# Kernel optimization log

Hardware: AMD Instinct MI355X
Metric: run time of the kernel (lower is better)

The kernel has to match this reference:

```python
import jax, jax.numpy as jnp
import numpy as np

H = 4096
IN = 512
OUT = 64


def setup_inputs() -> dict:
    key = jax.random.key(0)
    ks = jax.random.split(key, 10)
    return {
        "inp": jax.random.normal(ks[0], (1, IN), jnp.float32),
        "hidden": jax.random.normal(ks[1], (1, H), jnp.float32),
        "hebb": jax.random.normal(ks[2], (H, H), jnp.float32) * 0.01,
        "W_i2h": jax.random.normal(ks[3], (H, IN), jnp.float32) * (1.0 / np.sqrt(IN)),
        "b_i2h": jax.random.normal(ks[4], (H,), jnp.float32),
        "w": jax.random.uniform(ks[5], (H, H), jnp.float32) * 0.01,
        "plas": jax.random.uniform(ks[6], (H, H), jnp.float32) * 0.01,
        "learn": jnp.full((1,), 0.01, jnp.float32),
        "W_h2o": jax.random.normal(ks[7], (OUT, H), jnp.float32) * (1.0 / np.sqrt(H)),
        "b_h2o": jax.random.normal(ks[8], (OUT,), jnp.float32),
    }


def reference(inp, hidden, hebb, W_i2h, b_i2h, w, plas, learn, W_h2o, b_h2o):
    # plastic-Miconi, rule='hebb', activ='relu'
    # x = relu(i2h(input) + hidden @ (w + plas * hebb))   [1, H]
    pre = inp @ W_i2h.T + b_i2h + hidden @ (w + plas * hebb)
    x = jax.nn.relu(pre)
    # hebb <- (1 - learn) * hebb + learn * outer(hidden, x)   [H, H]
    hebb_new = (1.0 - learn) * hebb + learn * (hidden.T @ x)
    # output = tanh(h2o(x))   [1, OUT]
    out = jnp.tanh(x @ W_h2o.T + b_h2o)
    return out, x, hebb_new
```

## Files before the change

### kernel.cpp

```cpp
#include <hip/hip_runtime.h>
#include <math.h>

#define H 4096
#define INP 512
#define OUTN 64
#define H4 (H / 4)
#define SPLITS 1024
#define ROWS (H / SPLITS)

typedef float v4f __attribute__((ext_vector_type(4)));

__global__ __launch_bounds__(256) void k_partial(
    const float* __restrict__ hidden,
    const float* __restrict__ w,
    const float* __restrict__ plas,
    const float* __restrict__ hebb,
    float* __restrict__ partial)
{
    const int col4 = blockIdx.x * 256 + threadIdx.x;
    const int i0   = blockIdx.y * ROWS;
    const float4* __restrict__ w4 = (const float4*)w;
    const float4* __restrict__ p4 = (const float4*)plas;
    const float4* __restrict__ h4 = (const float4*)hebb;

    float4 wv[ROWS], pv[ROWS], hb[ROWS];
#pragma unroll
    for (int r = 0; r < ROWS; ++r) {
        const size_t idx = (size_t)(i0 + r) * H4 + col4;
        wv[r] = w4[idx];
        pv[r] = p4[idx];
        hb[r] = h4[idx];
    }
    float4 acc = make_float4(0.f, 0.f, 0.f, 0.f);
#pragma unroll
    for (int r = 0; r < ROWS; ++r) {
        const float hv = hidden[i0 + r];
        acc.x += hv * (wv[r].x + pv[r].x * hb[r].x);
        acc.y += hv * (wv[r].y + pv[r].y * hb[r].y);
        acc.z += hv * (wv[r].z + pv[r].z * hb[r].z);
        acc.w += hv * (wv[r].w + pv[r].w * hb[r].w);
    }
    ((float4*)partial)[(size_t)blockIdx.y * H4 + col4] = acc;
}

__global__ __launch_bounds__(256) void k_finish_x(
    const float* __restrict__ partial,
    const float* __restrict__ inp,
    const float* __restrict__ W_i2h,
    const float* __restrict__ b_i2h,
    float* __restrict__ x_out)
{
    const int t  = threadIdx.x;
    const int j0 = blockIdx.x * 16;
    const int jj = t & 15;
    const int sg = t >> 4;

    float sum = 0.f;
    for (int s = sg; s < SPLITS; s += 16)
        sum += partial[(size_t)s * H + j0 + jj];

    __shared__ float red[16][17];
    red[sg][jj] = sum;
    __syncthreads();

    const int wave = t >> 6;
    const int lane = t & 63;
    const float4* __restrict__ in4 = (const float4*)inp;

#pragma unroll
    for (int q = 0; q < 4; ++q) {
        const int jj2 = wave * 4 + q;
        const int j = j0 + jj2;
        const float4* __restrict__ row4 = (const float4*)(W_i2h + (size_t)j * INP);
        float d = 0.f;
#pragma unroll
        for (int k = 0; k < 2; ++k) {
            const float4 a = row4[lane + 64 * k];
            const float4 b = in4[lane + 64 * k];
            d += a.x * b.x + a.y * b.y + a.z * b.z + a.w * b.w;
        }
#pragma unroll
        for (int off = 32; off > 0; off >>= 1)
            d += __shfl_down(d, off, 64);
        if (lane == 0) {
            float tot = d + b_i2h[j];
#pragma unroll
            for (int g = 0; g < 16; ++g) tot += red[g][jj2];
            x_out[j] = tot > 0.f ? tot : 0.f;
        }
    }
}

__global__ __launch_bounds__(256) void k_hebb_out(
    const float* __restrict__ hebb,
    const float* __restrict__ hidden,
    const float* __restrict__ x,
    const float* __restrict__ learn,
    const float* __restrict__ W_h2o,
    const float* __restrict__ b_h2o,
    float* __restrict__ hebb_out,
    float* __restrict__ out)
{
    if (blockIdx.x < H) {
        const int i = blockIdx.x;
        const float lr = learn[0];
        const float om = 1.f - lr;
        const float coef = lr * hidden[i];
        const float4* __restrict__ hb4 = (const float4*)hebb;
        const float4* __restrict__ x4  = (const float4*)x;
        v4f* __restrict__ o4 = (v4f*)hebb_out;
        const size_t base = (size_t)i * H4;
#pragma unroll
        for (int c = threadIdx.x; c < H4; c += 256) {
            const float4 h  = hb4[base + c];
            const float4 xv = x4[c];
            v4f r;
            r.x = om * h.x + coef * xv.x;
            r.y = om * h.y + coef * xv.y;
            r.z = om * h.z + coef * xv.z;
            r.w = om * h.w + coef * xv.w;
            __builtin_nontemporal_store(r, &o4[base + c]);
        }
    } else {
        const int o = blockIdx.x - H;
        const float4* __restrict__ row4 = (const float4*)(W_h2o + (size_t)o * H);
        const float4* __restrict__ x4   = (const float4*)x;
        float sum = 0.f;
#pragma unroll
        for (int c = threadIdx.x; c < H4; c += 256) {
            const float4 a = row4[c];
            const float4 b = x4[c];
            sum += a.x * b.x + a.y * b.y + a.z * b.z + a.w * b.w;
        }
#pragma unroll
        for (int off = 32; off > 0; off >>= 1)
            sum += __shfl_down(sum, off, 64);
        __shared__ float red[4];
        const int lane = threadIdx.x & 63;
        if (lane == 0) red[threadIdx.x >> 6] = sum;
        __syncthreads();
        if (threadIdx.x == 0) {
            const float s = red[0] + red[1] + red[2] + red[3];
            out[o] = tanhf(s + b_h2o[o]);
        }
    }
}

extern "C" void kernel_launch(void* const* d_in, const int* in_sizes, int n_in,
                              void* d_out, int out_size, void* d_ws, size_t ws_size,
                              hipStream_t stream)
{
    const float* inp    = (const float*)d_in[0];
    const float* hidden = (const float*)d_in[1];
    const float* hebb   = (const float*)d_in[2];
    const float* W_i2h  = (const float*)d_in[3];
    const float* b_i2h  = (const float*)d_in[4];
    const float* w      = (const float*)d_in[5];
    const float* plas   = (const float*)d_in[6];
    const float* learn  = (const float*)d_in[7];
    const float* W_h2o  = (const float*)d_in[8];
    const float* b_h2o  = (const float*)d_in[9];

    float* out      = (float*)d_out;
    float* x        = out + OUTN;
    float* hebb_out = x + H;

    const size_t part_bytes = (size_t)SPLITS * H * sizeof(float);
    float* partial = (ws_size >= part_bytes) ? (float*)d_ws : hebb_out;

    k_partial<<<dim3(4, SPLITS), 256, 0, stream>>>(hidden, w, plas, hebb, partial);
    k_finish_x<<<256, 256, 0, stream>>>(partial, inp, W_i2h, b_i2h, x);
    k_hebb_out<<<H + OUTN, 256, 0, stream>>>(hebb, hidden, x, learn, W_h2o, b_h2o,
                                             hebb_out, out);
}
```

Before: 265.8 us.

## Fuse three kernels into one persistent kernel with grid barriers, keeping hebb in registers

Replaces the three launches with a single 1024-block persistent kernel that computes the partial matvec, synchronises through atomic grid barriers, finishes x, and then writes the hebb update. Each block keeps its 16 rows of hebb in registers, so hebb is not read a second time, and the partial buffer shrinks from 1024 to 256 splits. The cost is a memset plus two grid-wide spin barriers. Correctness relies on all 1024 blocks being resident at once, which the 4-blocks-per-SIMD launch bound is meant to ensure. A fallback keeps the old three-kernel path when the workspace is too small.

```diff
diff --git a/kernel.cpp b/kernel.cpp
--- a/kernel.cpp
+++ b/kernel.cpp
@@ -4,69 +4,189 @@
 #define H 4096
 #define INP 512
 #define OUTN 64
-#define H4 (H / 4)
-#define SPLITS 1024
-#define ROWS (H / SPLITS)
+#define H4 1024
+#define NBLK 1024
+#define SPLITS 256
+#define ROWS 16
 
 typedef float v4f __attribute__((ext_vector_type(4)));
 
-__global__ __launch_bounds__(256) void k_partial(
+__device__ __forceinline__ void grid_barrier(unsigned* ctr, unsigned target) {
+    __threadfence();
+    __syncthreads();
+    if (threadIdx.x == 0) {
+        atomicAdd(ctr, 1u);
+        while (atomicAdd(ctr, 0u) < target)
+            __builtin_amdgcn_s_sleep(2);
+    }
+    __syncthreads();
+    __threadfence();
+}
+
+__global__ __launch_bounds__(256, 4) void fused_rnn(
+    const float* __restrict__ inp,
     const float* __restrict__ hidden,
+    const float* __restrict__ hebb,
+    const float* __restrict__ W_i2h,
+    const float* __restrict__ b_i2h,
     const float* __restrict__ w,
     const float* __restrict__ plas,
-    const float* __restrict__ hebb,
-    float* __restrict__ partial)
-{
-    const int col4 = blockIdx.x * 256 + threadIdx.x;
-    const int i0   = blockIdx.y * ROWS;
+    const float* __restrict__ learn,
+    const float* __restrict__ W_h2o,
+    const float* __restrict__ b_h2o,
+    float* __restrict__ out,
+    float* __restrict__ x,
+    float* __restrict__ hebb_out,
+    float* __restrict__ partial,
+    unsigned* __restrict__ ctr)
+{
+    const int tid  = threadIdx.x;
+    const int bid  = blockIdx.x;
+    const int s    = bid >> 2;
+    const int col4 = (bid & 3) * 256 + tid;
+    const int i0   = s * ROWS;
+
     const float4* __restrict__ w4 = (const float4*)w;
     const float4* __restrict__ p4 = (const float4*)plas;
     const float4* __restrict__ h4 = (const float4*)hebb;
 
-    float4 wv[ROWS], pv[ROWS], hb[ROWS];
+    float4 hb[ROWS];
+    float4 acc = make_float4(0.f, 0.f, 0.f, 0.f);
 #pragma unroll
     for (int r = 0; r < ROWS; ++r) {
-        const size_t idx = (size_t)(i0 + r) * H4 + col4;
-        wv[r] = w4[idx];
-        pv[r] = p4[idx];
+        const int i = i0 + r;
+        const float hv = hidden[i];
+        const size_t idx = (size_t)i * H4 + col4;
+        const float4 wv = w4[idx];
+        const float4 pv = p4[idx];
         hb[r] = h4[idx];
-    }
+        acc.x += hv * (wv.x + pv.x * hb[r].x);
+        acc.y += hv * (wv.y + pv.y * hb[r].y);
+        acc.z += hv * (wv.z + pv.z * hb[r].z);
+        acc.w += hv * (wv.w + pv.w * hb[r].w);
+    }
+    ((float4*)partial)[(size_t)s * H4 + col4] = acc;
+
+    grid_barrier(ctr + 0, NBLK);
+
+    {
+        const int lane = tid & 63;
+        const int j = bid * 4 + (tid >> 6);
+        float sum = 0.f;
+#pragma unroll
+        for (int k = 0; k < 4; ++k)
+            sum += partial[(size_t)(lane + 64 * k) * H + j];
+
+        const float4* __restrict__ row4 = (const float4*)(W_i2h + (size_t)j * INP);
+        const float4* __restrict__ in4  = (const float4*)inp;
+#pragma unroll
+        for (int k = 0; k < 2; ++k) {
+            const float4 a = row4[lane + 64 * k];
+            const float4 b = in4[lane + 64 * k];
+            sum += a.x * b.x + a.y * b.y + a.z * b.z + a.w * b.w;
+        }
+#pragma unroll
+        for (int off = 32; off > 0; off >>= 1)
+            sum += __shfl_down(sum, off, 64);
+        if (lane == 0) {
+            const float pre = sum + b_i2h[j];
+            x[j] = pre > 0.f ? pre : 0.f;
+        }
+    }
+
+    grid_barrier(ctr + 1, NBLK);
+
+    {
+        const float lr = learn[0];
+        const float om = 1.f - lr;
+        const float4 xv = ((const float4*)x)[col4];
+        v4f* __restrict__ o4 = (v4f*)hebb_out;
+#pragma unroll
+        for (int r = 0; r < ROWS; ++r) {
+            const int i = i0 + r;
+            const float coef = lr * hidden[i];
+            v4f o;
+            o.x = om * hb[r].x + coef * xv.x;
+            o.y = om * hb[r].y + coef * xv.y;
+            o.z = om * hb[r].z + coef * xv.z;
+            o.w = om * hb[r].w + coef * xv.w;
+            __builtin_nontemporal_store(o, &o4[(size_t)i * H4 + col4]);
+        }
+    }
+
+    if (bid < OUTN) {
+        const int o = bid;
+        const float4* __restrict__ row4 = (const float4*)(W_h2o + (size_t)o * H);
+        const float4* __restrict__ x4   = (const float4*)x;
+        float sum = 0.f;
+#pragma unroll
+        for (int c = tid; c < H4; c += 256) {
+            const float4 a = row4[c];
+            const float4 b = x4[c];
+            sum += a.x * b.x + a.y * b.y + a.z * b.z + a.w * b.w;
+        }
+#pragma unroll
+        for (int off = 32; off > 0; off >>= 1)
+            sum += __shfl_down(sum, off, 64);
+        __shared__ float red[4];
+        const int lane = tid & 63;
+        if (lane == 0) red[tid >> 6] = sum;
+        __syncthreads();
+        if (tid == 0) {
+            const float ssum = red[0] + red[1] + red[2] + red[3];
+            out[o] = tanhf(ssum + b_h2o[o]);
+        }
+    }
+}
+
+#define FSPLITS 1024
+#define FROWS 4
+
+__global__ __launch_bounds__(256) void k_partial_fb(
+    const float* __restrict__ hidden, const float* __restrict__ w,
+    const float* __restrict__ plas, const float* __restrict__ hebb,
+    float* __restrict__ partial)
+{
+    const int col4 = blockIdx.x * 256 + threadIdx.x;
+    const int i0   = blockIdx.y * FROWS;
+    const float4* __restrict__ w4 = (const float4*)w;
+    const float4* __restrict__ p4 = (const float4*)plas;
+    const float4* __restrict__ h4 = (const float4*)hebb;
     float4 acc = make_float4(0.f, 0.f, 0.f, 0.f);
 #pragma unroll
-    for (int r = 0; r < ROWS; ++r) {
-        const float hv = hidden[i0 + r];
-        acc.x += hv * (wv[r].x + pv[r].x * hb[r].x);
-        acc.y += hv * (wv[r].y + pv[r].y * hb[r].y);
-        acc.z += hv * (wv[r].z + pv[r].z * hb[r].z);
-        acc.w += hv * (wv[r].w + pv[r].w * hb[r].w);
+    for (int r = 0; r < FROWS; ++r) {
+        const int i = i0 + r;
+        const float hv = hidden[i];
+        const size_t idx = (size_t)i * H4 + col4;
+        const float4 wv = w4[idx];
+        const float4 pv = p4[idx];
+        const float4 hbv = h4[idx];
+        acc.x += hv * (wv.x + pv.x * hbv.x);
+        acc.y += hv * (wv.y + pv.y * hbv.y);
+        acc.z += hv * (wv.z + pv.z * hbv.z);
+        acc.w += hv * (wv.w + pv.w * hbv.w);
     }
     ((float4*)partial)[(size_t)blockIdx.y * H4 + col4] = acc;
 }
 
-__global__ __launch_bounds__(256) void k_finish_x(
-    const float* __restrict__ partial,
-    const float* __restrict__ inp,
-    const float* __restrict__ W_i2h,
-    const float* __restrict__ b_i2h,
+__global__ __launch_bounds__(256) void k_finish_x_fb(
+    const float* __restrict__ partial, const float* __restrict__ inp,
+    const float* __restrict__ W_i2h, const float* __restrict__ b_i2h,
     float* __restrict__ x_out)
 {
     const int t  = threadIdx.x;
     const int j0 = blockIdx.x * 16;
     const int jj = t & 15;
     const int sg = t >> 4;
-
     float sum = 0.f;
-    for (int s = sg; s < SPLITS; s += 16)
+    for (int s = sg; s < FSPLITS; s += 16)
         sum += partial[(size_t)s * H + j0 + jj];
-
     __shared__ float red[16][17];
     red[sg][jj] = sum;
     __syncthreads();
-
     const int wave = t >> 6;
     const int lane = t & 63;
     const float4* __restrict__ in4 = (const float4*)inp;
-
 #pragma unroll
     for (int q = 0; q < 4; ++q) {
         const int jj2 = wave * 4 + q;
@@ -91,15 +211,11 @@
     }
 }
 
-__global__ __launch_bounds__(256) void k_hebb_out(
-    const float* __restrict__ hebb,
-    const float* __restrict__ hidden,
-    const float* __restrict__ x,
-    const float* __restrict__ learn,
-    const float* __restrict__ W_h2o,
-    const float* __restrict__ b_h2o,
-    float* __restrict__ hebb_out,
-    float* __restrict__ out)
+__global__ __launch_bounds__(256) void k_hebb_out_fb(
+    const float* __restrict__ hebb, const float* __restrict__ hidden,
+    const float* __restrict__ x, const float* __restrict__ learn,
+    const float* __restrict__ W_h2o, const float* __restrict__ b_h2o,
+    float* __restrict__ hebb_out, float* __restrict__ out)
 {
     if (blockIdx.x < H) {
         const int i = blockIdx.x;
@@ -112,13 +228,13 @@
         const size_t base = (size_t)i * H4;
 #pragma unroll
         for (int c = threadIdx.x; c < H4; c += 256) {
-            const float4 h  = hb4[base + c];
+            const float4 hv = hb4[base + c];
             const float4 xv = x4[c];
             v4f r;
-            r.x = om * h.x + coef * xv.x;
-            r.y = om * h.y + coef * xv.y;
-            r.z = om * h.z + coef * xv.z;
-            r.w = om * h.w + coef * xv.w;
+            r.x = om * hv.x + coef * xv.x;
+            r.y = om * hv.y + coef * xv.y;
+            r.z = om * hv.z + coef * xv.z;
+            r.w = om * hv.w + coef * xv.w;
             __builtin_nontemporal_store(r, &o4[base + c]);
         }
     } else {
@@ -140,8 +256,8 @@
         if (lane == 0) red[threadIdx.x >> 6] = sum;
         __syncthreads();
         if (threadIdx.x == 0) {
-            const float s = red[0] + red[1] + red[2] + red[3];
-            out[o] = tanhf(s + b_h2o[o]);
+            const float ssum = red[0] + red[1] + red[2] + red[3];
+            out[o] = tanhf(ssum + b_h2o[o]);
         }
     }
 }
@@ -165,11 +281,22 @@
     float* x        = out + OUTN;
     float* hebb_out = x + H;
 
+    const size_t ctr_bytes  = 256;
     const size_t part_bytes = (size_t)SPLITS * H * sizeof(float);
-    float* partial = (ws_size >= part_bytes) ? (float*)d_ws : hebb_out;
-
-    k_partial<<<dim3(4, SPLITS), 256, 0, stream>>>(hidden, w, plas, hebb, partial);
-    k_finish_x<<<256, 256, 0, stream>>>(partial, inp, W_i2h, b_i2h, x);
-    k_hebb_out<<<H + OUTN, 256, 0, stream>>>(hebb, hidden, x, learn, W_h2o, b_h2o,
-                                             hebb_out, out);
-}
+
+    if (ws_size >= ctr_bytes + part_bytes) {
+        unsigned* ctr  = (unsigned*)d_ws;
+        float* partial = (float*)((char*)d_ws + ctr_bytes);
+        hipMemsetAsync(ctr, 0, ctr_bytes, stream);
+        fused_rnn<<<NBLK, 256, 0, stream>>>(inp, hidden, hebb, W_i2h, b_i2h,
+                                            w, plas, learn, W_h2o, b_h2o,
+                                            out, x, hebb_out, partial, ctr);
+    } else {
+        const size_t fb_bytes = (size_t)FSPLITS * H * sizeof(float);
+        float* partial = (ws_size >= fb_bytes) ? (float*)d_ws : hebb_out;
+        k_partial_fb<<<dim3(4, FSPLITS), 256, 0, stream>>>(hidden, w, plas, hebb, partial);
+        k_finish_x_fb<<<256, 256, 0, stream>>>(partial, inp, W_i2h, b_i2h, x);
+        k_hebb_out_fb<<<H + OUTN, 256, 0, stream>>>(hebb, hidden, x, learn,
+                                                    W_h2o, b_h2o, hebb_out, out);
+    }
+}
```

Measured after the change: 850.7 us. +220.0%, slower.
